# Optimization experiments

Hardware: AMD Instinct MI355X
Metric: run time of the kernel (lower is better)

Reference implementation:

```python
import jax, jax.numpy as jnp
import numpy as np

D_MODEL = 256
N_HEADS = 4
WINDOW = 8
DECAY = 0.9
STEP_SIZE = 0.5


def _linear(x, w, b):
    # torch nn.Linear: y = x @ w.T + b, w: [out, in]
    return jnp.einsum('...i,oi->...o', x, w) + b


def _layernorm(x, scale, bias, eps=1e-5):
    mu = jnp.mean(x, axis=-1, keepdims=True)
    var = jnp.var(x, axis=-1, keepdims=True)
    return (x - mu) * jax.lax.rsqrt(var + eps) * scale + bias


def _ema(x, decay):
    # ema[t] = decay*ema[t-1] + (1-decay)*x[t], ema[-1]=0
    # (exactly the causal conv with weights (1-d)*d^i from the torch code)
    def step(c, xt):
        c = decay * c + (1.0 - decay) * xt
        return c, c
    _, ys = jax.lax.scan(step, jnp.zeros_like(x[:, 0]), jnp.swapaxes(x, 0, 1))
    return jnp.swapaxes(ys, 0, 1)


def setup_inputs() -> dict:
    key = jax.random.key(0)
    ks = iter(jax.random.split(key, 40))
    B, T, D = 8, 1024, D_MODEL
    s = 0.02
    inp = {
        'parallel_repr': jax.random.normal(next(ks), (B, T, D), jnp.float32),
        'sequential_state': jax.random.normal(next(ks), (B, D), jnp.float32),
        'trajectory_summary': jax.random.normal(next(ks), (B, D), jnp.float32),
        # MultiheadAttention params
        'in_proj_w': jax.random.normal(next(ks), (3 * D, D), jnp.float32) * s,
        'in_proj_b': jnp.zeros((3 * D,), jnp.float32),
        'out_proj_w': jax.random.normal(next(ks), (D, D), jnp.float32) * s,
        'out_proj_b': jnp.zeros((D,), jnp.float32),
        # depthwise causal conv (local history)
        'conv_w': jax.random.normal(next(ks), (D, 1, WINDOW), jnp.float32) * s,
        'conv_b': jnp.zeros((D,), jnp.float32),
        # parallel_to_sequential / sequential_to_parallel
        'p2s_w': jax.random.normal(next(ks), (D, D), jnp.float32) * s,
        'p2s_b': jnp.zeros((D,), jnp.float32),
        's2p_w': jax.random.normal(next(ks), (D, D), jnp.float32) * s,
        's2p_b': jnp.zeros((D,), jnp.float32),
        # transition MLP: 3D -> 2D -> D
        'trans_w1': jax.random.normal(next(ks), (2 * D, 3 * D), jnp.float32) * s,
        'trans_b1': jnp.zeros((2 * D,), jnp.float32),
        'trans_w2': jax.random.normal(next(ks), (D, 2 * D), jnp.float32) * s,
        'trans_b2': jnp.zeros((D,), jnp.float32),
        # FFN: D -> 4D -> D
        'ffn_w1': jax.random.normal(next(ks), (4 * D, D), jnp.float32) * s,
        'ffn_b1': jnp.zeros((4 * D,), jnp.float32),
        'ffn_w2': jax.random.normal(next(ks), (D, 4 * D), jnp.float32) * s,
        'ffn_b2': jnp.zeros((D,), jnp.float32),
        # LayerNorms
        'ln1_s': jnp.ones((D,), jnp.float32), 'ln1_b': jnp.zeros((D,), jnp.float32),
        'ln2_s': jnp.ones((D,), jnp.float32), 'ln2_b': jnp.zeros((D,), jnp.float32),
        'ln3_s': jnp.ones((D,), jnp.float32), 'ln3_b': jnp.zeros((D,), jnp.float32),
        'ln4_s': jnp.ones((D,), jnp.float32), 'ln4_b': jnp.zeros((D,), jnp.float32),
    }
    return inp


def _forward(parallel_repr, sequential_state,
             in_proj_w, in_proj_b, out_proj_w, out_proj_b,
             conv_w, conv_b, p2s_w, p2s_b, s2p_w, s2p_b,
             trans_w1, trans_b1, trans_w2, trans_b2,
             ffn_w1, ffn_b1, ffn_w2, ffn_b2,
             ln1_s, ln1_b, ln2_s, ln2_b, ln3_s, ln3_b, ln4_s, ln4_b):
    B, T, D = parallel_repr.shape
    H, hd = N_HEADS, D // N_HEADS

    # --- causal self-attention (nn.MultiheadAttention, batch_first) ---
    qkv = _linear(parallel_repr, in_proj_w, in_proj_b)
    q, k, v = jnp.split(qkv, 3, axis=-1)
    q = q.reshape(B, T, H, hd)
    k = k.reshape(B, T, H, hd)
    v = v.reshape(B, T, H, hd)
    scores = jnp.einsum('bqhd,bkhd->bhqk', q, k) / jnp.sqrt(jnp.asarray(hd, q.dtype))
    causal = jnp.triu(jnp.ones((T, T), bool), 1)
    scores = jnp.where(causal, jnp.finfo(scores.dtype).min, scores)
    attn = jax.nn.softmax(scores, axis=-1)
    attn_out = jnp.einsum('bhqk,bkhd->bqhd', attn, v).reshape(B, T, D)
    attn_out = _linear(attn_out, out_proj_w, out_proj_b)
    x = _layernorm(parallel_repr + attn_out, ln1_s, ln1_b)

    # --- depthwise causal conv (local history) ---
    xt = jnp.swapaxes(x, 1, 2)  # [B, D, T]
    xt_pad = jnp.pad(xt, ((0, 0), (0, 0), (WINDOW - 1, 0)))
    local = jax.lax.conv_general_dilated(
        xt_pad, conv_w, window_strides=(1,), padding='VALID',
        dimension_numbers=('NCH', 'OIH', 'NCH'), feature_group_count=D)
    local_history = jnp.swapaxes(local + conv_b[None, :, None], 1, 2)  # [B, T, D]

    # --- global EMA summary ---
    global_summary = _ema(x, DECAY)

    # --- transition deltas + cumsum state integration ---
    parallel_guidance = _linear(x, p2s_w, p2s_b)
    combined = jnp.concatenate([x + 0.3 * parallel_guidance, local_history, global_summary], axis=-1)
    h = jax.nn.gelu(_linear(combined, trans_w1, trans_b1), approximate=False)
    deltas = _linear(h, trans_w2, trans_b2)
    states = sequential_state[:, None, :] + jnp.cumsum(deltas, axis=1) * STEP_SIZE
    states = _layernorm(states, ln3_s, ln3_b)

    # --- FFN with sequential guidance ---
    seq_guidance = _linear(states, s2p_w, s2p_b)
    f = jax.nn.gelu(_linear(x + 0.3 * seq_guidance, ffn_w1, ffn_b1), approximate=False)
    ffn_out = _linear(f, ffn_w2, ffn_b2)
    x = _layernorm(x + ffn_out, ln2_s, ln2_b)

    final_sequential_state = _layernorm(states[:, -1, :], ln4_s, ln4_b)
    final_trajectory_summary = global_summary[:, -1, :]
    return x, final_sequential_state, final_trajectory_summary


def reference(parallel_repr, sequential_state, trajectory_summary,
              in_proj_w, in_proj_b, out_proj_w, out_proj_b,
              conv_w, conv_b, p2s_w, p2s_b, s2p_w, s2p_b,
              trans_w1, trans_b1, trans_w2, trans_b2,
              ffn_w1, ffn_b1, ffn_w2, ffn_b2,
              ln1_s, ln1_b, ln2_s, ln2_b, ln3_s, ln3_b, ln4_s, ln4_b):
    # trajectory_summary is accepted by the torch forward but never used.
    return _forward(parallel_repr, sequential_state,
                    in_proj_w, in_proj_b, out_proj_w, out_proj_b,
                    conv_w, conv_b, p2s_w, p2s_b, s2p_w, s2p_b,
                    trans_w1, trans_b1, trans_w2, trans_b2,
                    ffn_w1, ffn_b1, ffn_w2, ffn_b2,
                    ln1_s, ln1_b, ln2_s, ln2_b, ln3_s, ln3_b, ln4_s, ln4_b)
```

## Files before the change

### kernel.cpp

```cpp
#include <hip/hip_runtime.h>
#include <math.h>

typedef unsigned short u16;
typedef __attribute__((ext_vector_type(8))) short bf16x8;
typedef __attribute__((ext_vector_type(4))) float f32x4;

#define D_MODEL 256
#define T_SZ 1024
constexpr size_t S_ELT = (size_t)8192 * 256;
constexpr size_t MB = 1024 * 1024;

constexpr size_t OFF_QKV = 0;
constexpr size_t OFF_ATTN = 12 * MB;
constexpr size_t OFF_F = 0;
constexpr size_t OFF_X = 16 * MB;
constexpr size_t OFF_COMB = 24 * MB;
constexpr size_t OFF_FB = 36 * MB;
constexpr size_t OFF_H = 44 * MB;
constexpr size_t OFF_XBF = 48 * MB;
constexpr size_t OFF_WB = 52 * MB;
constexpr size_t OFF_SCR1 = 55 * MB;
constexpr size_t OFF_SCR2 = 55 * MB + 262144;
constexpr size_t OFF_B1E = 55 * MB + 524288;

constexpr int WB_INPROJ = 0;
constexpr int WB_OUTPROJ = 196608;
constexpr int WB_P2S = 262144;
constexpr int WB_S2P = 327680;
constexpr int WB_T1 = 393216;
constexpr int WB_T2 = 786432;
constexpr int WB_F1 = 917504;
constexpr int WB_F2 = 1179648;
constexpr int WB_TOTAL = 1441792;
constexpr int PR_TOTAL = 2097152;

__device__ __forceinline__ u16 f2bf(float f) {
  unsigned int u = __float_as_uint(f);
  u += 0x7fff + ((u >> 16) & 1);
  return (u16)(u >> 16);
}
__device__ __forceinline__ float bf2f(u16 s) {
  return __uint_as_float(((unsigned int)s) << 16);
}

__device__ __forceinline__ void glds16(const u16* g, u16* l) {
  __builtin_amdgcn_global_load_lds(
      (const __attribute__((address_space(1))) void*)g,
      (__attribute__((address_space(3))) void*)l, 16, 0, 0);
}

__global__ __launch_bounds__(256)
void wconv_kernel(const float* w0, const float* w1, const float* w2,
                  const float* w3, const float* w4, const float* w5,
                  const float* w6, const float* w7, const float* pr,
                  u16* __restrict__ wb, u16* __restrict__ prb) {
  const int idx4 = (blockIdx.x * 256 + threadIdx.x) * 4;
  if (idx4 < WB_TOTAL) {
    const int offs[9] = {WB_INPROJ, WB_OUTPROJ, WB_P2S,  WB_S2P, WB_T1,
                         WB_T2,     WB_F1,      WB_F2,   WB_TOTAL};
    const float* srcs[8] = {w0, w1, w2, w3, w4, w5, w6, w7};
    int seg = 0;
    while (idx4 >= offs[seg + 1]) ++seg;
    float4 v = *(const float4*)(srcs[seg] + (idx4 - offs[seg]));
    unsigned int lo = (unsigned int)f2bf(v.x) | ((unsigned int)f2bf(v.y) << 16);
    unsigned int hi = (unsigned int)f2bf(v.z) | ((unsigned int)f2bf(v.w) << 16);
    *(uint2*)(wb + idx4) = make_uint2(lo, hi);
  } else {
    const int i4 = idx4 - WB_TOTAL;
    if (i4 < PR_TOTAL) {
      float4 v = *(const float4*)(pr + i4);
      unsigned int lo = (unsigned int)f2bf(v.x) | ((unsigned int)f2bf(v.y) << 16);
      unsigned int hi = (unsigned int)f2bf(v.z) | ((unsigned int)f2bf(v.w) << 16);
      *(uint2*)(prb + i4) = make_uint2(lo, hi);
    }
  }
}

__global__ __launch_bounds__(256)
void wfold_kernel(const float* __restrict__ t1, const float* __restrict__ p2s,
                  const float* __restrict__ t1b, const float* __restrict__ p2sb,
                  u16* __restrict__ wt1, float* __restrict__ b1e) {
  __shared__ float trow[8][256];
  const int o0 = blockIdx.x * 8;
  const int k = threadIdx.x;
#pragma unroll
  for (int r = 0; r < 8; ++r)
    trow[r][k] = t1[(size_t)(o0 + r) * 768 + k];
  __syncthreads();
  float acc[8] = {};
  float bacc[8] = {};
  for (int i = 0; i < 256; ++i) {
    const float pv = p2s[(size_t)i * 256 + k];
    const float pbv = p2sb[i];
#pragma unroll
    for (int r = 0; r < 8; ++r) {
      acc[r] = fmaf(trow[r][i], pv, acc[r]);
      bacc[r] = fmaf(trow[r][i], pbv, bacc[r]);
    }
  }
#pragma unroll
  for (int r = 0; r < 8; ++r)
    wt1[(size_t)(o0 + r) * 768 + k] = f2bf(trow[r][k] + 0.3f * acc[r]);
  if (k == 0) {
#pragma unroll
    for (int r = 0; r < 8; ++r)
      b1e[o0 + r] = t1b[o0 + r] + 0.3f * bacc[r];
  }
}

enum { EPI_NONE = 0, EPI_GELU = 1, EPI_ADDSCALE = 2 };

template <int EPI, int BM, int BN, bool OUTBF, bool VSPLIT>
__global__ __launch_bounds__(256, 4)
void mgemm(const u16* __restrict__ A, int lda,
           const u16* __restrict__ Wb, int K, const float* __restrict__ bias,
           void* __restrict__ Cv, int ldc, int col_off,
           const float* __restrict__ addsrc, u16* __restrict__ vt) {
  __shared__ u16 As[BM * 64];
  __shared__ u16 Bs[BN * 64];
  const int tid = threadIdx.x;
  const int w = tid >> 6, lane = tid & 63;
  const int ln = lane & 15, quad = lane >> 4;
  const int m0 = blockIdx.x * BM;
  const int n0 = blockIdx.y * BN;
  constexpr int MT = (BM == 128) ? 2 : 1;
  const int wm = w * (MT * 16);
  constexpr int wn = 0;
  constexpr int APW = BM / 64;
  constexpr int BPW = BN / 64;

  f32x4 acc[MT][4] = {};

  const int grow = lane >> 2;
  const int gk8 = (lane & 3) * 8;

  for (int k0 = 0; k0 < K; k0 += 64) {
#pragma unroll
    for (int s = 0; s < 2; ++s) {
#pragma unroll
      for (int p = 0; p < APW; ++p) {
        const int g = w * APW + p;
        glds16(A + (size_t)(m0 + g * 16 + grow) * lda + k0 + s * 32 + gk8,
               As + s * BM * 32 + g * 512);
      }
#pragma unroll
      for (int p = 0; p < BPW; ++p) {
        const int g = w * BPW + p;
        glds16(Wb + (size_t)(n0 + g * 16 + grow) * K + k0 + s * 32 + gk8,
               Bs + s * BN * 32 + g * 512);
      }
    }
    __syncthreads();
#pragma unroll
    for (int s = 0; s < 2; ++s) {
      const u16* abase = As + s * BM * 32 + (wm >> 4) * 512 + ln * 32 + quad * 8;
      const u16* bbase = Bs + s * BN * 32 + ln * 32 + quad * 8;
      bf16x8 af[MT], bv[4];
#pragma unroll
      for (int i = 0; i < MT; ++i) af[i] = *(const bf16x8*)(abase + i * 512);
#pragma unroll
      for (int j = 0; j < 4; ++j) bv[j] = *(const bf16x8*)(bbase + j * 512);
#pragma unroll
      for (int i = 0; i < MT; ++i)
#pragma unroll
        for (int j = 0; j < 4; ++j)
          acc[i][j] = __builtin_amdgcn_mfma_f32_16x16x32_bf16(af[i], bv[j],
                                                              acc[i][j], 0, 0, 0);
    }
    __syncthreads();
  }

#pragma unroll
  for (int i = 0; i < MT; ++i)
#pragma unroll
    for (int j = 0; j < 4; ++j) {
      const int col = n0 + wn + j * 16 + ln;
      const float bsv = bias[col];
      const int row0 = m0 + wm + i * 16 + quad * 4;
      float vals[4];
#pragma unroll
      for (int r = 0; r < 4; ++r) {
        float v = acc[i][j][r] + bsv;
        if (EPI == EPI_GELU) v = 0.5f * v * (1.0f + erff(v * 0.70710678f));
        if (EPI == EPI_ADDSCALE)
          v = addsrc[(size_t)(row0 + r) * 256 + col] + 0.3f * v;
        vals[r] = v;
      }
      if (VSPLIT && col >= 512) {
        ushort4 pk;
        pk.x = f2bf(vals[0]); pk.y = f2bf(vals[1]);
        pk.z = f2bf(vals[2]); pk.w = f2bf(vals[3]);
        *(ushort4*)(vt + (size_t)((row0 >> 10) * 256 + (col - 512)) * T_SZ +
                    (row0 & 1023)) = pk;
      } else if (OUTBF) {
#pragma unroll
        for (int r = 0; r < 4; ++r)
          ((u16*)Cv)[(size_t)(row0 + r) * ldc + col_off + col] = f2bf(vals[r]);
      } else {
#pragma unroll
        for (int r = 0; r < 4; ++r)
          ((float*)Cv)[(size_t)(row0 + r) * ldc + col_off + col] = vals[r];
      }
    }
}

template <bool WRITE_BF>
__global__ __launch_bounds__(256, 4)
void mgemm_ln16(const u16* __restrict__ A, const u16* __restrict__ Wb, int K,
                const float* __restrict__ bias, const float* __restrict__ addsrc,
                const float* __restrict__ g, const float* __restrict__ bb,
                float* __restrict__ outf, u16* __restrict__ outbf, int bfldc) {
  __shared__ u16 As[2 * 512];
  __shared__ u16 Bs[2 * 8192];
  __shared__ float tS1[4][16], tS2[4][16];
  const int tid = threadIdx.x;
  const int w = tid >> 6, lane = tid & 63;
  const int ln = lane & 15, quad = lane >> 4;
  const int m0 = blockIdx.x * 16;
  const int grow = lane >> 2;
  const int gk8 = (lane & 3) * 8;

  f32x4 acc[4] = {};

  for (int k0 = 0; k0 < K; k0 += 64) {
    if (w < 2)
      glds16(A + (size_t)(m0 + grow) * K + k0 + w * 32 + gk8, As + w * 512);
#pragma unroll
    for (int p = 0; p < 8; ++p) {
      const int idx = w * 8 + p;
      const int s = idx >> 4, gg = idx & 15;
      glds16(Wb + (size_t)(gg * 16 + grow) * K + k0 + s * 32 + gk8,
             Bs + s * 8192 + gg * 512);
    }
    __syncthreads();
#pragma unroll
    for (int s = 0; s < 2; ++s) {
      const bf16x8 af = *(const bf16x8*)(As + s * 512 + ln * 32 + quad * 8);
      const u16* bbase = Bs + s * 8192 + (w * 4) * 512 + ln * 32 + quad * 8;
#pragma unroll
      for (int j = 0; j < 4; ++j) {
        bf16x8 bv = *(const bf16x8*)(bbase + j * 512);
        acc[j] = __builtin_amdgcn_mfma_f32_16x16x32_bf16(af, bv, acc[j], 0, 0, 0);
      }
    }
    __syncthreads();
  }

  const int row0 = m0 + quad * 4;
  float s1[4] = {}, s2[4] = {};
#pragma unroll
  for (int j = 0; j < 4; ++j) {
    const int col = w * 64 + j * 16 + ln;
    const float bsv = bias[col];
#pragma unroll
    for (int r = 0; r < 4; ++r) {
      float v = acc[j][r] + bsv + addsrc[(size_t)(row0 + r) * 256 + col];
      acc[j][r] = v;
      s1[r] += v;
      s2[r] += v * v;
    }
  }
#pragma unroll
  for (int r = 0; r < 4; ++r) {
#pragma unroll
    for (int o = 8; o > 0; o >>= 1) {
      s1[r] += __shfl_xor(s1[r], o);
      s2[r] += __shfl_xor(s2[r], o);
    }
  }
  if (ln == 0) {
#pragma unroll
    for (int r = 0; r < 4; ++r) {
      tS1[w][quad * 4 + r] = s1[r];
      tS2[w][quad * 4 + r] = s2[r];
    }
  }
  __syncthreads();
  float mean[4], inv[4];
#pragma unroll
  for (int r = 0; r < 4; ++r) {
    const int qr = quad * 4 + r;
    const float S1 = tS1[0][qr] + tS1[1][qr] + tS1[2][qr] + tS1[3][qr];
    const float S2 = tS2[0][qr] + tS2[1][qr] + tS2[2][qr] + tS2[3][qr];
    mean[r] = S1 * (1.f / 256.f);
    const float var = S2 * (1.f / 256.f) - mean[r] * mean[r];
    inv[r] = rsqrtf(var + 1e-5f);
  }
#pragma unroll
  for (int j = 0; j < 4; ++j) {
    const int col = w * 64 + j * 16 + ln;
    const float gc = g[col], bc = bb[col];
#pragma unroll
    for (int r = 0; r < 4; ++r) {
      const float y = (acc[j][r] - mean[r]) * inv[r] * gc + bc;
      outf[(size_t)(row0 + r) * 256 + col] = y;
      if (WRITE_BF) outbf[(size_t)(row0 + r) * bfldc + col] = f2bf(y);
    }
  }
}

__global__ __launch_bounds__(256)
void attn_flash(const u16* __restrict__ qkv, const u16* __restrict__ vt,
                u16* __restrict__ outp) {
  __shared__ u16 Ks[2][4096];
  __shared__ u16 Vs[2][4096];
  __shared__ u16 Ps[4][16][72];
  const int tid = threadIdx.x;
  const int w = tid >> 6, lane = tid & 63;
  const int ln = lane & 15, quad = lane >> 4, kq8 = quad * 8;
  const int bid = blockIdx.x;
  const int r0 = bid & 255;
  int bh = r0 >> 4;
  int p = r0 & 15;
  if (bid >> 8) { bh += 16; p = 15 - p; }
  const int qt = p * 4 + w;
  const int q0 = qt * 16;
  const int b = bh >> 2, h = bh & 3;
  const u16* base = qkv + (size_t)b * T_SZ * 768;
  const u16* kbase = base + 256 + h * 64;
  const u16* vbase = vt + (size_t)bh * 64 * T_SZ;
  const int grow = lane >> 2;
  const int gk8 = (lane & 3) * 8;

  bf16x8 qf[2];
#pragma unroll
  for (int ks = 0; ks < 2; ++ks)
    qf[ks] = *(const bf16x8*)(base + (size_t)(q0 + ln) * 768 + h * 64 +
                              ks * 32 + kq8);
  const short ob = (short)0x3F80;
  const bf16x8 ones = {ob, ob, ob, ob, ob, ob, ob, ob};

  const int nt = p + 1;

#define STAGE_KV(jt, buf)                                                     \
  {                                                                           \
    const int c0s = (jt) * 64;                                                \
    const int isV = w >> 1, ss = w & 1;                                       \
    _Pragma("unroll") for (int pg = 0; pg < 4; ++pg) {                        \
      if (!isV)                                                               \
        glds16(kbase + (size_t)(c0s + pg * 16 + grow) * 768 + ss * 32 + gk8,  \
               &Ks[buf][ss * 2048 + pg * 512]);                               \
      else                                                                    \
        glds16(vbase + (size_t)(pg * 16 + grow) * T_SZ + c0s + ss * 32 + gk8, \
               &Vs[buf][ss * 2048 + pg * 512]);                               \
    }                                                                         \
  }

  f32x4 O[4] = {};
  f32x4 l_acc = {};
  int cur = 0;
  STAGE_KV(0, 0);
  for (int jt = 0; jt < nt; ++jt) {
    __syncthreads();
    if (jt + 1 < nt) STAGE_KV(jt + 1, cur ^ 1);
    const int c0 = jt * 64;
    f32x4 sv[4] = {};
#pragma unroll
    for (int ks = 0; ks < 2; ++ks)
#pragma unroll
      for (int j = 0; j < 4; ++j) {
        bf16x8 kf = *(const bf16x8*)&Ks[cur][ks * 2048 + j * 512 + ln * 32 + kq8];
        sv[j] = __builtin_amdgcn_mfma_f32_16x16x32_bf16(qf[ks], kf, sv[j], 0, 0, 0);
      }
    const bool need_mask = (jt == nt - 1);
#pragma unroll
    for (int j = 0; j < 4; ++j)
#pragma unroll
      for (int r = 0; r < 4; ++r) {
        float pv = __expf(sv[j][r] * 0.125f);
        if (need_mask && (c0 + j * 16 + ln > q0 + quad * 4 + r)) pv = 0.f;
        Ps[w][quad * 4 + r][j * 16 + ln] = f2bf(pv);
      }
#pragma unroll
    for (int ks = 0; ks < 2; ++ks) {
      bf16x8 pf = *(const bf16x8*)&Ps[w][ln][ks * 32 + kq8];
      l_acc = __builtin_amdgcn_mfma_f32_16x16x32_bf16(pf, ones, l_acc, 0, 0, 0);
#pragma unroll
      for (int j = 0; j < 4; ++j) {
        bf16x8 vf = *(const bf16x8*)&Vs[cur][ks * 2048 + j * 512 + ln * 32 + kq8];
        O[j] = __builtin_amdgcn_mfma_f32_16x16x32_bf16(pf, vf, O[j], 0, 0, 0);
      }
    }
    cur ^= 1;
  }
#undef STAGE_KV

  u16* op = outp + (size_t)b * T_SZ * 256;
#pragma unroll
  for (int r = 0; r < 4; ++r) {
    const float inv = 1.f / l_acc[r];
#pragma unroll
    for (int j = 0; j < 4; ++j)
      op[(size_t)(q0 + quad * 4 + r) * 256 + h * 64 + j * 16 + ln] =
          f2bf(O[j][r] * inv);
  }
}

__device__ __forceinline__ void block_reduce_2(float& a, float& q, float* tmp) {
#pragma unroll
  for (int o = 32; o > 0; o >>= 1) {
    a += __shfl_down(a, o);
    q += __shfl_down(q, o);
  }
  const int lane = threadIdx.x & 63, wid = threadIdx.x >> 6;
  if (lane == 0) { tmp[wid] = a; tmp[4 + wid] = q; }
  __syncthreads();
  a = tmp[0] + tmp[1] + tmp[2] + tmp[3];
  q = tmp[4] + tmp[5] + tmp[6] + tmp[7];
  __syncthreads();
}

__device__ __forceinline__ float ln_finish(float v, float s1, float s2,
                                           float g, float bb) {
  float mean = s1 * (1.f / 256.f);
  float var = s2 * (1.f / 256.f) - mean * mean;
  return (v - mean) * rsqrtf(var + 1e-5f) * g + bb;
}

__global__ __launch_bounds__(256)
void emaconv_kernel(const float* __restrict__ x, const float* __restrict__ cw,
                    const float* __restrict__ cb, u16* __restrict__ comb,
                    float* __restrict__ scr) {
  const int bc = blockIdx.x;
  const int b = bc >> 5, ch = bc & 31;
  const int d = threadIdx.x;
  const int t0 = ch * 32;
  float wreg[8];
#pragma unroll
  for (int j = 0; j < 8; ++j) wreg[j] = cw[d * 8 + j];
  const float bias = cb[d];
  float xw[8];
#pragma unroll
  for (int j = 0; j < 7; ++j) {
    const int ts = t0 - 7 + j;
    xw[j] = (ts >= 0) ? x[(size_t)(b * T_SZ + ts) * 256 + d] : 0.f;
  }
  float c = 0.f;
#pragma unroll
  for (int tl = 0; tl < 32; ++tl) {
    const size_t row = (size_t)(b * T_SZ + t0 + tl);
    xw[7] = x[row * 256 + d];
    float conv = bias;
#pragma unroll
    for (int j = 0; j < 8; ++j) conv = fmaf(xw[j], wreg[j], conv);
    c = 0.9f * c + 0.1f * xw[7];
    comb[row * 768 + 256 + d] = f2bf(conv);
    comb[row * 768 + 512 + d] = f2bf(c);
#pragma unroll
    for (int j = 0; j < 7; ++j) xw[j] = xw[j + 1];
  }
  scr[(size_t)bc * 256 + d] = c;
}

__global__ __launch_bounds__(256)
void ema_b_kernel(float* __restrict__ scr) {
  const int b = blockIdx.x, d = threadIdx.x;
  const float q32 = 0.03433683820292512f;
  float carry = 0.f;
  for (int ch = 0; ch < 32; ++ch) {
    const size_t idx = (size_t)(b * 32 + ch) * 256 + d;
    float e = scr[idx];
    scr[idx] = carry;
    carry = e + q32 * carry;
  }
}

__global__ __launch_bounds__(256)
void ema_c_kernel(u16* __restrict__ comb, const float* __restrict__ scr,
                  float* __restrict__ fts) {
  const int row = blockIdx.x;
  const int b = row >> 10, t = row & 1023;
  const int d = threadIdx.x;
  const int ch = t >> 5, tl = t & 31;
  float carry = scr[(size_t)(b * 32 + ch) * 256 + d];
  float l = bf2f(comb[(size_t)row * 768 + 512 + d]);
  float y = fmaf(__powf(0.9f, (float)(tl + 1)), carry, l);
  comb[(size_t)row * 768 + 512 + d] = f2bf(y);
  if (t == 1023) fts[b * 256 + d] = y;
}

__global__ __launch_bounds__(256)
void cs_a_kernel(float* __restrict__ deltas, float* __restrict__ scr) {
  const int bc = blockIdx.x;
  const int b = bc >> 5, ch = bc & 31;
  const int d = threadIdx.x;
  const int t0 = ch * 32;
  float c = 0.f;
  for (int tl = 0; tl < 32; ++tl) {
    const size_t idx = (size_t)(b * T_SZ + t0 + tl) * 256 + d;
    c += deltas[idx];
    deltas[idx] = c;
  }
  scr[(size_t)bc * 256 + d] = c;
}

__global__ __launch_bounds__(256)
void cs_b_kernel(float* __restrict__ scr) {
  const int b = blockIdx.x, d = threadIdx.x;
  float carry = 0.f;
  for (int ch = 0; ch < 32; ++ch) {
    const size_t idx = (size_t)(b * 32 + ch) * 256 + d;
    float e = scr[idx];
    scr[idx] = carry;
    carry += e;
  }
}

__global__ __launch_bounds__(256)
void ln3_states_kernel(const float* __restrict__ deltas, const float* __restrict__ scr,
                       const float* __restrict__ seq, const float* __restrict__ g3,
                       const float* __restrict__ b3, const float* __restrict__ g4,
                       const float* __restrict__ b4, u16* __restrict__ st,
                       float* __restrict__ fss) {
  __shared__ float tmp[8];
  const int row = blockIdx.x;
  const int b = row >> 10, t = row & 1023;
  const int d = threadIdx.x;
  float v = seq[b * 256 + d] +
            0.5f * (deltas[(size_t)row * 256 + d] +
                    scr[(size_t)(b * 32 + (t >> 5)) * 256 + d]);
  float a = v, q = v * v;
  block_reduce_2(a, q, tmp);
  const float y = ln_finish(v, a, q, g3[d], b3[d]);
  st[(size_t)row * 256 + d] = f2bf(y);
  if (t == 1023) {
    float a2 = y, q2 = y * y;
    block_reduce_2(a2, q2, tmp);
    fss[b * 256 + d] = ln_finish(y, a2, q2, g4[d], b4[d]);
  }
}

extern "C" void kernel_launch(void* const* d_in, const int* in_sizes, int n_in,
                              void* d_out, int out_size, void* d_ws,
                              size_t ws_size, hipStream_t stream) {
  (void)in_sizes; (void)n_in; (void)out_size; (void)ws_size;
  const float* parallel_repr = (const float*)d_in[0];
  const float* sequential_state = (const float*)d_in[1];
  const float* in_proj_b = (const float*)d_in[4];
  const float* out_proj_b = (const float*)d_in[6];
  const float* conv_w = (const float*)d_in[7];
  const float* conv_b = (const float*)d_in[8];
  const float* p2s_w_f = (const float*)d_in[9];
  const float* p2s_b = (const float*)d_in[10];
  const float* s2p_b = (const float*)d_in[12];
  const float* trans_w1_f = (const float*)d_in[13];
  const float* trans_b1 = (const float*)d_in[14];
  const float* trans_b2 = (const float*)d_in[16];
  const float* ffn_b1 = (const float*)d_in[18];
  const float* ffn_b2 = (const float*)d_in[20];
  const float* ln1_s = (const float*)d_in[21];
  const float* ln1_b = (const float*)d_in[22];
  const float* ln2_s = (const float*)d_in[23];
  const float* ln2_b = (const float*)d_in[24];
  const float* ln3_s = (const float*)d_in[25];
  const float* ln3_b = (const float*)d_in[26];
  const float* ln4_s = (const float*)d_in[27];
  const float* ln4_b = (const float*)d_in[28];

  char* ws = (char*)d_ws;
  u16* qkv_bf = (u16*)(ws + OFF_QKV);
  u16* attn_bf = (u16*)(ws + OFF_ATTN);
  u16* states_bf = (u16*)(ws + OFF_ATTN);
  u16* f_bf = (u16*)(ws + OFF_F);
  float* x = (float*)(ws + OFF_X);
  u16* comb = (u16*)(ws + OFF_COMB);
  u16* pr_bf = (u16*)(ws + OFF_COMB);
  float* fbuf = (float*)(ws + OFF_FB);
  u16* vt = (u16*)(ws + OFF_H);
  u16* h_bf = (u16*)(ws + OFF_H);
  u16* ffn_in = (u16*)(ws + OFF_XBF);
  u16* wb = (u16*)(ws + OFF_WB);
  float* scr1 = (float*)(ws + OFF_SCR1);
  float* scr2 = (float*)(ws + OFF_SCR2);
  float* b1e = (float*)(ws + OFF_B1E);
  float* out = (float*)d_out;
  float* out_fss = out + S_ELT;
  float* out_fts = out + S_ELT + 2048;

  const dim3 blk(256);

  wconv_kernel<<<3456, blk, 0, stream>>>(
      (const float*)d_in[3], (const float*)d_in[5], (const float*)d_in[9],
      (const float*)d_in[11], (const float*)d_in[13], (const float*)d_in[15],
      (const float*)d_in[17], (const float*)d_in[19], parallel_repr, wb, pr_bf);
  wfold_kernel<<<64, blk, 0, stream>>>(trans_w1_f, p2s_w_f, trans_b1, p2s_b,
                                       wb + WB_T1, b1e);
  mgemm<EPI_NONE, 128, 64, true, true><<<dim3(64, 12), blk, 0, stream>>>(
      pr_bf, 256, wb + WB_INPROJ, 256, in_proj_b, qkv_bf, 768, 0, nullptr, vt);
  attn_flash<<<512, blk, 0, stream>>>(qkv_bf, vt, attn_bf);
  mgemm_ln16<true><<<512, blk, 0, stream>>>(
      attn_bf, wb + WB_OUTPROJ, 256, out_proj_b, parallel_repr, ln1_s, ln1_b,
      x, comb, 768);
  emaconv_kernel<<<256, blk, 0, stream>>>(x, conv_w, conv_b, comb, scr1);
  ema_b_kernel<<<8, blk, 0, stream>>>(scr1);
  ema_c_kernel<<<8192, blk, 0, stream>>>(comb, scr1, out_fts);
  mgemm<EPI_GELU, 128, 64, true, false><<<dim3(64, 8), blk, 0, stream>>>(
      comb, 768, wb + WB_T1, 768, b1e, h_bf, 512, 0, nullptr, nullptr);
  mgemm<EPI_NONE, 64, 64, false, false><<<dim3(128, 4), blk, 0, stream>>>(
      h_bf, 512, wb + WB_T2, 512, trans_b2, fbuf, 256, 0, nullptr, nullptr);
  cs_a_kernel<<<256, blk, 0, stream>>>(fbuf, scr2);
  cs_b_kernel<<<8, blk, 0, stream>>>(scr2);
  ln3_states_kernel<<<8192, blk, 0, stream>>>(fbuf, scr2, sequential_state,
                                              ln3_s, ln3_b, ln4_s, ln4_b,
                                              states_bf, out_fss);
  mgemm<EPI_ADDSCALE, 64, 64, true, false><<<dim3(128, 4), blk, 0, stream>>>(
      states_bf, 256, wb + WB_S2P, 256, s2p_b, ffn_in, 256, 0, x, nullptr);
  mgemm<EPI_GELU, 128, 64, true, false><<<dim3(64, 16), blk, 0, stream>>>(
      ffn_in, 256, wb + WB_F1, 256, ffn_b1, f_bf, 1024, 0, nullptr, nullptr);
  mgemm_ln16<false><<<512, blk, 0, stream>>>(
      f_bf, wb + WB_F2, 1024, ffn_b2, x, ln2_s, ln2_b, out, nullptr, 256);
}
```

Before: 260.4 us.

## Fold s2p projection into FFN1 weights and double-buffer LDS in GEMMs

Removes the separate s2p GEMM with its add-and-scale epilogue. It precomputes a folded weight 0.3·F1·s2p and a folded bias in the weight-fold kernel. FFN1 then runs a split-K GEMM over the bf16 x columns of comb plus the states buffer. Both GEMM kernels also get double-buffered LDS, so the next K tile is staged while the current one is consumed. This adds a barrier before the LayerNorm reduction scratch. The cost is doubled LDS per block, which can reduce occupancy, especially in the LayerNorm GEMM whose B tile is now 64KB. The folded weights are also rounded to bf16.

```diff
diff --git a/kernel.cpp b/kernel.cpp
--- a/kernel.cpp
+++ b/kernel.cpp
@@ -17,12 +17,7 @@
 constexpr size_t OFF_COMB = 24 * MB;
 constexpr size_t OFF_FB = 36 * MB;
 constexpr size_t OFF_H = 44 * MB;
-constexpr size_t OFF_XBF = 48 * MB;
 constexpr size_t OFF_WB = 52 * MB;
-constexpr size_t OFF_SCR1 = 55 * MB;
-constexpr size_t OFF_SCR2 = 55 * MB + 262144;
-constexpr size_t OFF_B1E = 55 * MB + 524288;
-
 constexpr int WB_INPROJ = 0;
 constexpr int WB_OUTPROJ = 196608;
 constexpr int WB_P2S = 262144;
@@ -33,6 +28,11 @@
 constexpr int WB_F2 = 1179648;
 constexpr int WB_TOTAL = 1441792;
 constexpr int PR_TOTAL = 2097152;
+constexpr size_t OFF_B1E = OFF_WB + (size_t)WB_TOTAL * 2;
+constexpr size_t OFF_B1E2 = OFF_B1E + 4096;
+constexpr size_t OFF_WC2 = 55 * MB;
+constexpr size_t OFF_SCR1 = 55 * MB + 524288;
+constexpr size_t OFF_SCR2 = 55 * MB + 786432;
 
 __device__ __forceinline__ u16 f2bf(float f) {
   unsigned int u = __float_as_uint(f);
@@ -79,45 +79,65 @@
 __global__ __launch_bounds__(256)
 void wfold_kernel(const float* __restrict__ t1, const float* __restrict__ p2s,
                   const float* __restrict__ t1b, const float* __restrict__ p2sb,
-                  u16* __restrict__ wt1, float* __restrict__ b1e) {
+                  const float* __restrict__ f1, const float* __restrict__ s2p,
+                  const float* __restrict__ f1b, const float* __restrict__ s2pb,
+                  u16* __restrict__ wt1, float* __restrict__ b1e,
+                  u16* __restrict__ wc2, float* __restrict__ b1e2) {
   __shared__ float trow[8][256];
-  const int o0 = blockIdx.x * 8;
+  const int blk = blockIdx.x;
   const int k = threadIdx.x;
+  const bool t1role = blk < 64;
+  const int o0 = t1role ? blk * 8 : (blk - 64) * 8;
+  const float* wsrc = t1role ? t1 : f1;
+  const int wstride = t1role ? 768 : 256;
+  const float* psrc = t1role ? p2s : s2p;
+  const float* pbsrc = t1role ? p2sb : s2pb;
 #pragma unroll
   for (int r = 0; r < 8; ++r)
-    trow[r][k] = t1[(size_t)(o0 + r) * 768 + k];
+    trow[r][k] = wsrc[(size_t)(o0 + r) * wstride + k];
   __syncthreads();
   float acc[8] = {};
   float bacc[8] = {};
   for (int i = 0; i < 256; ++i) {
-    const float pv = p2s[(size_t)i * 256 + k];
-    const float pbv = p2sb[i];
+    const float pv = psrc[(size_t)i * 256 + k];
+    const float pbv = pbsrc[i];
 #pragma unroll
     for (int r = 0; r < 8; ++r) {
       acc[r] = fmaf(trow[r][i], pv, acc[r]);
       bacc[r] = fmaf(trow[r][i], pbv, bacc[r]);
     }
   }
-#pragma unroll
-  for (int r = 0; r < 8; ++r)
-    wt1[(size_t)(o0 + r) * 768 + k] = f2bf(trow[r][k] + 0.3f * acc[r]);
-  if (k == 0) {
+  if (t1role) {
 #pragma unroll
     for (int r = 0; r < 8; ++r)
-      b1e[o0 + r] = t1b[o0 + r] + 0.3f * bacc[r];
-  }
-}
-
-enum { EPI_NONE = 0, EPI_GELU = 1, EPI_ADDSCALE = 2 };
-
-template <int EPI, int BM, int BN, bool OUTBF, bool VSPLIT>
+      wt1[(size_t)(o0 + r) * 768 + k] = f2bf(trow[r][k] + 0.3f * acc[r]);
+    if (k == 0) {
+#pragma unroll
+      for (int r = 0; r < 8; ++r)
+        b1e[o0 + r] = t1b[o0 + r] + 0.3f * bacc[r];
+    }
+  } else {
+#pragma unroll
+    for (int r = 0; r < 8; ++r)
+      wc2[(size_t)(o0 + r) * 256 + k] = f2bf(0.3f * acc[r]);
+    if (k == 0) {
+#pragma unroll
+      for (int r = 0; r < 8; ++r)
+        b1e2[o0 + r] = f1b[o0 + r] + 0.3f * bacc[r];
+    }
+  }
+}
+
+enum { EPI_NONE = 0, EPI_GELU = 1 };
+
+template <int EPI, int BM, int BN, bool OUTBF, bool VSPLIT, bool SPLIT>
 __global__ __launch_bounds__(256, 4)
-void mgemm(const u16* __restrict__ A, int lda,
-           const u16* __restrict__ Wb, int K, const float* __restrict__ bias,
-           void* __restrict__ Cv, int ldc, int col_off,
-           const float* __restrict__ addsrc, u16* __restrict__ vt) {
-  __shared__ u16 As[BM * 64];
-  __shared__ u16 Bs[BN * 64];
+void mgemm(const u16* __restrict__ A, int lda, const u16* __restrict__ A2,
+           const u16* __restrict__ Wb, int ldb, const u16* __restrict__ B2,
+           int K, const float* __restrict__ bias, void* __restrict__ Cv,
+           int ldc, int col_off, u16* __restrict__ vt) {
+  __shared__ u16 As[2 * BM * 64];
+  __shared__ u16 Bs[2 * BN * 64];
   const int tid = threadIdx.x;
   const int w = tid >> 6, lane = tid & 63;
   const int ln = lane & 15, quad = lane >> 4;
@@ -125,7 +145,6 @@
   const int n0 = blockIdx.y * BN;
   constexpr int MT = (BM == 128) ? 2 : 1;
   const int wm = w * (MT * 16);
-  constexpr int wn = 0;
   constexpr int APW = BM / 64;
   constexpr int BPW = BN / 64;
 
@@ -134,27 +153,38 @@
   const int grow = lane >> 2;
   const int gk8 = (lane & 3) * 8;
 
+#define STAGE_MM(k0s, buf)                                                    \
+  {                                                                           \
+    const u16* Ag; const u16* Bg; int as_, bs_, kk;                           \
+    if (!SPLIT || (k0s) < 256) {                                              \
+      Ag = A; as_ = lda; Bg = Wb; bs_ = ldb; kk = (k0s);                      \
+    } else {                                                                  \
+      Ag = A2; as_ = 256; Bg = B2; bs_ = 256; kk = (k0s)-256;                 \
+    }                                                                         \
+    _Pragma("unroll") for (int s = 0; s < 2; ++s) {                           \
+      _Pragma("unroll") for (int p = 0; p < APW; ++p) {                       \
+        const int g = w * APW + p;                                            \
+        glds16(Ag + (size_t)(m0 + g * 16 + grow) * as_ + kk + s * 32 + gk8,   \
+               As + (buf) * (BM * 64) + s * BM * 32 + g * 512);               \
+      }                                                                       \
+      _Pragma("unroll") for (int p = 0; p < BPW; ++p) {                       \
+        const int g = w * BPW + p;                                            \
+        glds16(Bg + (size_t)(n0 + g * 16 + grow) * bs_ + kk + s * 32 + gk8,   \
+               Bs + (buf) * (BN * 64) + s * BN * 32 + g * 512);               \
+      }                                                                       \
+    }                                                                         \
+  }
+
+  int cur = 0;
+  STAGE_MM(0, 0);
   for (int k0 = 0; k0 < K; k0 += 64) {
+    __syncthreads();
+    if (k0 + 64 < K) STAGE_MM(k0 + 64, cur ^ 1);
 #pragma unroll
     for (int s = 0; s < 2; ++s) {
-#pragma unroll
-      for (int p = 0; p < APW; ++p) {
-        const int g = w * APW + p;
-        glds16(A + (size_t)(m0 + g * 16 + grow) * lda + k0 + s * 32 + gk8,
-               As + s * BM * 32 + g * 512);
-      }
-#pragma unroll
-      for (int p = 0; p < BPW; ++p) {
-        const int g = w * BPW + p;
-        glds16(Wb + (size_t)(n0 + g * 16 + grow) * K + k0 + s * 32 + gk8,
-               Bs + s * BN * 32 + g * 512);
-      }
-    }
-    __syncthreads();
-#pragma unroll
-    for (int s = 0; s < 2; ++s) {
-      const u16* abase = As + s * BM * 32 + (wm >> 4) * 512 + ln * 32 + quad * 8;
-      const u16* bbase = Bs + s * BN * 32 + ln * 32 + quad * 8;
+      const u16* abase =
+          As + cur * (BM * 64) + s * BM * 32 + (wm >> 4) * 512 + ln * 32 + quad * 8;
+      const u16* bbase = Bs + cur * (BN * 64) + s * BN * 32 + ln * 32 + quad * 8;
       bf16x8 af[MT], bv[4];
 #pragma unroll
       for (int i = 0; i < MT; ++i) af[i] = *(const bf16x8*)(abase + i * 512);
@@ -167,14 +197,15 @@
           acc[i][j] = __builtin_amdgcn_mfma_f32_16x16x32_bf16(af[i], bv[j],
                                                               acc[i][j], 0, 0, 0);
     }
-    __syncthreads();
-  }
+    cur ^= 1;
+  }
+#undef STAGE_MM
 
 #pragma unroll
   for (int i = 0; i < MT; ++i)
 #pragma unroll
     for (int j = 0; j < 4; ++j) {
-      const int col = n0 + wn + j * 16 + ln;
+      const int col = n0 + j * 16 + ln;
       const float bsv = bias[col];
       const int row0 = m0 + wm + i * 16 + quad * 4;
       float vals[4];
@@ -182,8 +213,6 @@
       for (int r = 0; r < 4; ++r) {
         float v = acc[i][j][r] + bsv;
         if (EPI == EPI_GELU) v = 0.5f * v * (1.0f + erff(v * 0.70710678f));
-        if (EPI == EPI_ADDSCALE)
-          v = addsrc[(size_t)(row0 + r) * 256 + col] + 0.3f * v;
         vals[r] = v;
       }
       if (VSPLIT && col >= 512) {
@@ -210,8 +239,8 @@
                 const float* __restrict__ bias, const float* __restrict__ addsrc,
                 const float* __restrict__ g, const float* __restrict__ bb,
                 float* __restrict__ outf, u16* __restrict__ outbf, int bfldc) {
-  __shared__ u16 As[2 * 512];
-  __shared__ u16 Bs[2 * 8192];
+  __shared__ u16 As[2 * 1024];
+  __shared__ u16 Bs[2 * 16384];
   __shared__ float tS1[4][16], tS2[4][16];
   const int tid = threadIdx.x;
   const int w = tid >> 6, lane = tid & 63;
@@ -222,29 +251,39 @@
 
   f32x4 acc[4] = {};
 
+#define STAGE_LN(k0s, buf)                                                    \
+  {                                                                           \
+    if (w < 2)                                                                \
+      glds16(A + (size_t)(m0 + grow) * K + (k0s) + w * 32 + gk8,              \
+             As + (buf) * 1024 + w * 512);                                    \
+    _Pragma("unroll") for (int p = 0; p < 8; ++p) {                           \
+      const int idx = w * 8 + p;                                              \
+      const int s = idx >> 4, gg = idx & 15;                                  \
+      glds16(Wb + (size_t)(gg * 16 + grow) * K + (k0s) + s * 32 + gk8,        \
+             Bs + (buf) * 16384 + s * 8192 + gg * 512);                       \
+    }                                                                         \
+  }
+
+  int cur = 0;
+  STAGE_LN(0, 0);
   for (int k0 = 0; k0 < K; k0 += 64) {
-    if (w < 2)
-      glds16(A + (size_t)(m0 + grow) * K + k0 + w * 32 + gk8, As + w * 512);
-#pragma unroll
-    for (int p = 0; p < 8; ++p) {
-      const int idx = w * 8 + p;
-      const int s = idx >> 4, gg = idx & 15;
-      glds16(Wb + (size_t)(gg * 16 + grow) * K + k0 + s * 32 + gk8,
-             Bs + s * 8192 + gg * 512);
-    }
     __syncthreads();
+    if (k0 + 64 < K) STAGE_LN(k0 + 64, cur ^ 1);
 #pragma unroll
     for (int s = 0; s < 2; ++s) {
-      const bf16x8 af = *(const bf16x8*)(As + s * 512 + ln * 32 + quad * 8);
-      const u16* bbase = Bs + s * 8192 + (w * 4) * 512 + ln * 32 + quad * 8;
+      const bf16x8 af =
+          *(const bf16x8*)(As + cur * 1024 + s * 512 + ln * 32 + quad * 8);
+      const u16* bbase =
+          Bs + cur * 16384 + s * 8192 + (w * 4) * 512 + ln * 32 + quad * 8;
 #pragma unroll
       for (int j = 0; j < 4; ++j) {
         bf16x8 bv = *(const bf16x8*)(bbase + j * 512);
         acc[j] = __builtin_amdgcn_mfma_f32_16x16x32_bf16(af, bv, acc[j], 0, 0, 0);
       }
     }
-    __syncthreads();
-  }
+    cur ^= 1;
+  }
+#undef STAGE_LN
 
   const int row0 = m0 + quad * 4;
   float s1[4] = {}, s2[4] = {};
@@ -268,6 +307,7 @@
       s2[r] += __shfl_xor(s2[r], o);
     }
   }
+  __syncthreads();
   if (ln == 0) {
 #pragma unroll
     for (int r = 0; r < 4; ++r) {
@@ -542,10 +582,12 @@
   const float* conv_b = (const float*)d_in[8];
   const float* p2s_w_f = (const float*)d_in[9];
   const float* p2s_b = (const float*)d_in[10];
+  const float* s2p_w_f = (const float*)d_in[11];
   const float* s2p_b = (const float*)d_in[12];
   const float* trans_w1_f = (const float*)d_in[13];
   const float* trans_b1 = (const float*)d_in[14];
   const float* trans_b2 = (const float*)d_in[16];
+  const float* ffn_w1_f = (const float*)d_in[17];
   const float* ffn_b1 = (const float*)d_in[18];
   const float* ffn_b2 = (const float*)d_in[20];
   const float* ln1_s = (const float*)d_in[21];
@@ -568,11 +610,12 @@
   float* fbuf = (float*)(ws + OFF_FB);
   u16* vt = (u16*)(ws + OFF_H);
   u16* h_bf = (u16*)(ws + OFF_H);
-  u16* ffn_in = (u16*)(ws + OFF_XBF);
   u16* wb = (u16*)(ws + OFF_WB);
+  u16* wc2 = (u16*)(ws + OFF_WC2);
   float* scr1 = (float*)(ws + OFF_SCR1);
   float* scr2 = (float*)(ws + OFF_SCR2);
   float* b1e = (float*)(ws + OFF_B1E);
+  float* b1e2 = (float*)(ws + OFF_B1E2);
   float* out = (float*)d_out;
   float* out_fss = out + S_ELT;
   float* out_fts = out + S_ELT + 2048;
@@ -583,10 +626,12 @@
       (const float*)d_in[3], (const float*)d_in[5], (const float*)d_in[9],
       (const float*)d_in[11], (const float*)d_in[13], (const float*)d_in[15],
       (const float*)d_in[17], (const float*)d_in[19], parallel_repr, wb, pr_bf);
-  wfold_kernel<<<64, blk, 0, stream>>>(trans_w1_f, p2s_w_f, trans_b1, p2s_b,
-                                       wb + WB_T1, b1e);
-  mgemm<EPI_NONE, 128, 64, true, true><<<dim3(64, 12), blk, 0, stream>>>(
-      pr_bf, 256, wb + WB_INPROJ, 256, in_proj_b, qkv_bf, 768, 0, nullptr, vt);
+  wfold_kernel<<<192, blk, 0, stream>>>(trans_w1_f, p2s_w_f, trans_b1, p2s_b,
+                                        ffn_w1_f, s2p_w_f, ffn_b1, s2p_b,
+                                        wb + WB_T1, b1e, wc2, b1e2);
+  mgemm<EPI_NONE, 128, 64, true, true, false><<<dim3(64, 12), blk, 0, stream>>>(
+      pr_bf, 256, nullptr, wb + WB_INPROJ, 256, nullptr, 256, in_proj_b,
+      qkv_bf, 768, 0, vt);
   attn_flash<<<512, blk, 0, stream>>>(qkv_bf, vt, attn_bf);
   mgemm_ln16<true><<<512, blk, 0, stream>>>(
       attn_bf, wb + WB_OUTPROJ, 256, out_proj_b, parallel_repr, ln1_s, ln1_b,
@@ -594,19 +639,20 @@
   emaconv_kernel<<<256, blk, 0, stream>>>(x, conv_w, conv_b, comb, scr1);
   ema_b_kernel<<<8, blk, 0, stream>>>(scr1);
   ema_c_kernel<<<8192, blk, 0, stream>>>(comb, scr1, out_fts);
-  mgemm<EPI_GELU, 128, 64, true, false><<<dim3(64, 8), blk, 0, stream>>>(
-      comb, 768, wb + WB_T1, 768, b1e, h_bf, 512, 0, nullptr, nullptr);
-  mgemm<EPI_NONE, 64, 64, false, false><<<dim3(128, 4), blk, 0, stream>>>(
-      h_bf, 512, wb + WB_T2, 512, trans_b2, fbuf, 256, 0, nullptr, nullptr);
+  mgemm<EPI_GELU, 128, 64, true, false, false><<<dim3(64, 8), blk, 0, stream>>>(
+      comb, 768, nullptr, wb + WB_T1, 768, nullptr, 768, b1e, h_bf, 512, 0,
+      nullptr);
+  mgemm<EPI_NONE, 64, 64, false, false, false><<<dim3(128, 4), blk, 0, stream>>>(
+      h_bf, 512, nullptr, wb + WB_T2, 512, nullptr, 512, trans_b2, fbuf, 256,
+      0, nullptr);
   cs_a_kernel<<<256, blk, 0, stream>>>(fbuf, scr2);
   cs_b_kernel<<<8, blk, 0, stream>>>(scr2);
   ln3_states_kernel<<<8192, blk, 0, stream>>>(fbuf, scr2, sequential_state,
                                               ln3_s, ln3_b, ln4_s, ln4_b,
                                               states_bf, out_fss);
-  mgemm<EPI_ADDSCALE, 64, 64, true, false><<<dim3(128, 4), blk, 0, stream>>>(
-      states_bf, 256, wb + WB_S2P, 256, s2p_b, ffn_in, 256, 0, x, nullptr);
-  mgemm<EPI_GELU, 128, 64, true, false><<<dim3(64, 16), blk, 0, stream>>>(
-      ffn_in, 256, wb + WB_F1, 256, ffn_b1, f_bf, 1024, 0, nullptr, nullptr);
+  mgemm<EPI_GELU, 128, 64, true, false, true><<<dim3(64, 16), blk, 0, stream>>>(
+      comb, 768, states_bf, wb + WB_F1, 256, wc2, 512, b1e2, f_bf, 1024, 0,
+      nullptr);
   mgemm_ln16<false><<<512, blk, 0, stream>>>(
       f_bf, wb + WB_F2, 1024, ffn_b2, x, ln2_s, ln2_b, out, nullptr, 256);
 }
```

After: 263.3 us. About the same (+1.1%).
